# Kernel tuning notes

Measured on AMD Instinct MI355X. Metric: run time of the kernel, lower is better.

The kernel has to match this reference:

```python
import jax, jax.numpy as jnp
from jax import lax
import numpy as np

B, T = 16, 96      # sentences per batch, EDUs per document
K = 64             # kcluster
D = 768            # BERT_DIM
H = 400            # n_lstm_hidden
L = 3              # n_lstm_layers
M = 500            # n_mlp_arc
NEG = -1e9


def setup_inputs() -> dict:
    key = jax.random.key(0)
    ks = jax.random.split(key, 16)
    s = 0.1
    return {
        "embed_table": jax.random.normal(ks[0], (K, D), jnp.float32) * s,
        "multinomial": jax.random.normal(ks[1], (K, K), jnp.float32) * s,
        "wih0": jax.random.normal(ks[2], (2, 4 * H, D), jnp.float32) * s,
        "wih": jax.random.normal(ks[3], (L - 1, 2, 4 * H, 2 * H), jnp.float32) * s,
        "whh": jax.random.normal(ks[4], (L, 2, 4 * H, H), jnp.float32) * s,
        "b": jax.random.normal(ks[5], (L, 2, 4 * H), jnp.float32) * s,
        "mlp_h_w": jax.random.normal(ks[6], (M, 2 * H), jnp.float32) * s,
        "mlp_h_b": jax.random.normal(ks[7], (M,), jnp.float32) * s,
        "mlp_d_w": jax.random.normal(ks[8], (M, 2 * H), jnp.float32) * s,
        "mlp_d_b": jax.random.normal(ks[9], (M,), jnp.float32) * s,
        "biaffine_w": jax.random.normal(ks[10], (M, M), jnp.float32) * s,
        "kmeans_labels": jax.random.randint(ks[11], (B, T), 0, K),
        "heads": jax.random.randint(ks[12], (B, T - 1), 0, T),
    }


def _lse(x, axis):
    m = jnp.max(x, axis=axis, keepdims=True)
    return jnp.squeeze(m, axis) + jnp.log(jnp.sum(jnp.exp(x - m), axis=axis))


def _lstm_dir(x, Wih, Whh, bias, reverse):
    # x: [B, T, in] -> [B, T, H]; torch gate order i,f,g,o; bias = b_ih + b_hh
    xs = jnp.swapaxes(x, 0, 1)

    def step(carry, xt):
        h, c = carry
        g = xt @ Wih.T + h @ Whh.T + bias
        i, f, gg, o = jnp.split(g, 4, axis=-1)
        c = jax.nn.sigmoid(f) * c + jax.nn.sigmoid(i) * jnp.tanh(gg)
        h = jax.nn.sigmoid(o) * jnp.tanh(c)
        return (h, c), h

    z = jnp.zeros((x.shape[0], Whh.shape[1]), x.dtype)
    _, hs = lax.scan(step, (z, z), xs, reverse=reverse)
    return jnp.swapaxes(hs, 0, 1)


def _inside(s):
    # Eisner first-order inside algorithm in the log semiring.
    # s[h, d] = log-score of arc h -> d. Returns log-partition.
    n = s.shape[0]
    eye = jnp.eye(n, dtype=bool)
    C_r = jnp.where(eye, 0.0, NEG)  # complete, head on left
    C_l = jnp.where(eye, 0.0, NEG)  # complete, head on right
    I_r = jnp.full((n, n), NEG)
    I_l = jnp.full((n, n), NEG)
    for w in range(1, n):
        i = jnp.arange(n - w)
        j = i + w
        r = jnp.arange(w)
        ii = i[:, None]
        # incomplete spans: split k in [i, j-1]
        inc = _lse(C_r[ii, ii + r] + C_l[ii + r + 1, j[:, None]], axis=1)
        I_r = I_r.at[i, j].set(inc + s[i, j])
        I_l = I_l.at[i, j].set(inc + s[j, i])
        # complete right: split k in [i+1, j]
        rr = jnp.arange(1, w + 1)
        cr = _lse(I_r[ii, ii + rr] + C_r[ii + rr, j[:, None]], axis=1)
        C_r = C_r.at[i, j].set(cr)
        # complete left: split k in [i, j-1]
        cl = _lse(C_l[ii, ii + r] + I_l[ii + r, j[:, None]], axis=1)
        C_l = C_l.at[i, j].set(cl)
    return C_r[0, n - 1]


def reference(embed_table, multinomial, wih0, wih, whh, b, mlp_h_w, mlp_h_b,
              mlp_d_w, mlp_d_b, biaffine_w, kmeans_labels, heads):
    # embed lookup of kmeans cluster labels (word_embed=False branch)
    x = embed_table[kmeans_labels]  # [B, T, D]
    # 3-layer BiLSTM (eval mode: dropout = identity)
    for l in range(L):
        Wf = wih0[0] if l == 0 else wih[l - 1, 0]
        Wb = wih0[1] if l == 0 else wih[l - 1, 1]
        hf = _lstm_dir(x, Wf, whh[l, 0], b[l, 0], reverse=False)
        hb = _lstm_dir(x, Wb, whh[l, 1], b[l, 1], reverse=True)
        x = jnp.concatenate([hf, hb], axis=-1)  # [B, T, 2H]
    # arc MLPs (LeakyReLU(0.1) as in the biaffine parser MLP)
    arc_h = jax.nn.leaky_relu(x @ mlp_h_w.T + mlp_h_b, 0.1)
    arc_d = jax.nn.leaky_relu(x @ mlp_d_w.T + mlp_d_b, 0.1)
    # biaffine arc scores: s_arc[b, dep, head]
    s_arc = jnp.einsum('bxi,ij,byj->bxy', arc_d, biaffine_w, arc_h)
    # encoder_p[b, head, dep] = log_softmax over heads, then permute(0,2,1)
    p = jnp.swapaxes(jax.nn.log_softmax(s_arc, axis=-1), 1, 2)
    # reconstruction weight from raw multinomial over cluster labels
    rec = multinomial[kmeans_labels[:, :, None], kmeans_labels[:, None, :]]
    joint = p + rec  # [B, T, T]
    # score of the given (gold) tree: heads[b, d-1] -> d for deps 1..T-1
    deps = jnp.arange(1, T)
    best_score = joint[jnp.arange(B)[:, None], heads, deps[None, :]].sum(axis=1)
    # Eisner log-partition per sentence over encoder_p
    partition = jax.vmap(_inside)(p)
    # supervised loss: mean of -(best_score - partition)
    return jnp.mean(partition - best_score)
```

## Files before the change

kernel.cpp:

```cpp
#include <hip/hip_runtime.h>
#include <cmath>

#define DEV __device__ __forceinline__


#define NBLK_LSTM 400

DEV float wred_max(float v){ for(int o=32;o;o>>=1) v=fmaxf(v,__shfl_xor(v,o)); return v; }
DEV float wred_sum(float v){ for(int o=32;o;o>>=1) v+=__shfl_xor(v,o); return v; }
DEV float sigf(float x){ return 1.f/(1.f+__expf(-x)); }

DEV float agent_ld(const float* p){
  return __hip_atomic_load(p, __ATOMIC_RELAXED, __HIP_MEMORY_SCOPE_AGENT);
}
DEV void agent_st(float* p, float v){
  __hip_atomic_store(p, v, __ATOMIC_RELAXED, __HIP_MEMORY_SCOPE_AGENT);
}

__global__ __launch_bounds__(256) void embed_kern(const float* __restrict__ tab,
                                                  const int* __restrict__ labels,
                                                  float* __restrict__ x0){
  long idx = (long)blockIdx.x*256 + threadIdx.x;
  if (idx >= 1536L*768) return;
  int m = (int)(idx/768), d = (int)(idx%768);
  x0[idx] = tab[(long)labels[m]*768 + d];
}

__global__ __launch_bounds__(256) void trans_sq(const float* __restrict__ w,
                                                float* __restrict__ wt){
  int idx = blockIdx.x*256 + threadIdx.x;
  if (idx >= 250000) return;
  int j = idx/500, i = idx%500;
  wt[idx] = w[(long)i*500 + j];
}

__global__ __launch_bounds__(256) void gemm_abt(const float* __restrict__ A,
                                                const float* __restrict__ Bm,
                                                float* __restrict__ C,
                                                const float* __restrict__ bias,
                                                int M, int N, int K,
                                                long sA, long sB, long sC, int leaky){
  A  += (long)blockIdx.z * sA;
  Bm += (long)blockIdx.z * sB;
  C  += (long)blockIdx.z * sC;
  __shared__ float As[16][68];
  __shared__ float Bs[16][68];
  int tid = threadIdx.x;
  int tx = tid & 15, ty = tid >> 4;
  int m0 = blockIdx.x * 64, n0 = blockIdx.y * 64;
  int lrow = tid >> 2, lc = (tid & 3) * 4;
  float acc[4][4] = {};
  for (int k0 = 0; k0 < K; k0 += 16) {
    #pragma unroll
    for (int u = 0; u < 4; u++) {
      int k = k0 + lc + u;
      int am = m0 + lrow;
      As[lc+u][lrow] = (am < M && k < K) ? A[(long)am*K + k] : 0.f;
      int bn = n0 + lrow;
      Bs[lc+u][lrow] = (bn < N && k < K) ? Bm[(long)bn*K + k] : 0.f;
    }
    __syncthreads();
    #pragma unroll
    for (int kk = 0; kk < 16; kk++) {
      float a[4], bb[4];
      #pragma unroll
      for (int u=0;u<4;u++){ a[u]=As[kk][ty*4+u]; bb[u]=Bs[kk][tx*4+u]; }
      #pragma unroll
      for (int i=0;i<4;i++)
        #pragma unroll
        for (int j=0;j<4;j++) acc[i][j] = fmaf(a[i], bb[j], acc[i][j]);
    }
    __syncthreads();
  }
  #pragma unroll
  for (int i=0;i<4;i++){
    int m = m0 + ty*4 + i;
    if (m >= M) continue;
    #pragma unroll
    for (int j=0;j<4;j++){
      int n = n0 + tx*4 + j;
      if (n >= N) continue;
      float v = acc[i][j];
      if (bias) v += bias[n];
      if (leaky) v = v > 0.f ? v : 0.1f*v;
      C[(long)m*N + n] = v;
    }
  }
}

__global__ __launch_bounds__(256) void gemm128(const float* __restrict__ A,
                                               const float* __restrict__ Bm,
                                               float* __restrict__ C,
                                               const float* __restrict__ bias,
                                               int M, int N, int K, int leaky){
  __shared__ float As[16][132];
  __shared__ float Bs[16][132];
  int tid = threadIdx.x;
  int tx = tid & 15, ty = tid >> 4;
  int m0 = blockIdx.x*128, n0 = blockIdx.y*128;
  int lr = tid >> 1, lq = (tid & 1)*8;
  const float* Arow = A + (size_t)(m0+lr)*K + lq;
  const float* Brow = Bm + (size_t)(n0+lr)*K + lq;
  bool bok = (n0 + lr) < N;
  float acc[8][8] = {};
  for (int k0 = 0; k0 < K; k0 += 16){
    if (k0 + 16 <= K){
      float4 a0 = *(const float4*)(Arow + k0);
      float4 a1 = *(const float4*)(Arow + k0 + 4);
      float4 b0 = {0,0,0,0}, b1 = {0,0,0,0};
      if (bok){ b0 = *(const float4*)(Brow + k0); b1 = *(const float4*)(Brow + k0 + 4); }
      As[lq+0][lr]=a0.x; As[lq+1][lr]=a0.y; As[lq+2][lr]=a0.z; As[lq+3][lr]=a0.w;
      As[lq+4][lr]=a1.x; As[lq+5][lr]=a1.y; As[lq+6][lr]=a1.z; As[lq+7][lr]=a1.w;
      Bs[lq+0][lr]=b0.x; Bs[lq+1][lr]=b0.y; Bs[lq+2][lr]=b0.z; Bs[lq+3][lr]=b0.w;
      Bs[lq+4][lr]=b1.x; Bs[lq+5][lr]=b1.y; Bs[lq+6][lr]=b1.z; Bs[lq+7][lr]=b1.w;
    } else {
      #pragma unroll
      for (int u = 0; u < 8; u++){
        int k = k0 + lq + u;
        As[lq+u][lr] = (k < K) ? Arow[k0+u] : 0.f;
        Bs[lq+u][lr] = (bok && k < K) ? Brow[k0+u] : 0.f;
      }
    }
    __syncthreads();
    #pragma unroll
    for (int kk = 0; kk < 16; kk++){
      float4 a0 = *(const float4*)&As[kk][ty*8];
      float4 a1 = *(const float4*)&As[kk][ty*8+4];
      float4 b0 = *(const float4*)&Bs[kk][tx*8];
      float4 b1 = *(const float4*)&Bs[kk][tx*8+4];
      float av[8] = {a0.x,a0.y,a0.z,a0.w,a1.x,a1.y,a1.z,a1.w};
      float bv[8] = {b0.x,b0.y,b0.z,b0.w,b1.x,b1.y,b1.z,b1.w};
      #pragma unroll
      for (int i=0;i<8;i++)
        #pragma unroll
        for (int j=0;j<8;j++) acc[i][j] = fmaf(av[i], bv[j], acc[i][j]);
    }
    __syncthreads();
  }
  bool full = (n0 + 128 <= N);
  #pragma unroll
  for (int i = 0; i < 8; i++){
    int m = m0 + ty*8 + i;
    float* Crow = C + (size_t)m*N;
    if (full){
      float4 v0, v1;
      float* p0 = &v0.x; float* p1 = &v1.x;
      #pragma unroll
      for (int j = 0; j < 4; j++){
        int n = n0 + tx*8 + j;
        float v = acc[i][j];
        if (bias) v += bias[n];
        if (leaky) v = v > 0.f ? v : 0.1f*v;
        p0[j] = v;
      }
      #pragma unroll
      for (int j = 4; j < 8; j++){
        int n = n0 + tx*8 + j;
        float v = acc[i][j];
        if (bias) v += bias[n];
        if (leaky) v = v > 0.f ? v : 0.1f*v;
        p1[j-4] = v;
      }
      *(float4*)(Crow + n0 + tx*8)     = v0;
      *(float4*)(Crow + n0 + tx*8 + 4) = v1;
    } else {
      #pragma unroll
      for (int j = 0; j < 8; j++){
        int n = n0 + tx*8 + j;
        if (n < N){
          float v = acc[i][j];
          if (bias) v += bias[n];
          if (leaky) v = v > 0.f ? v : 0.1f*v;
          Crow[n] = v;
        }
      }
    }
  }
}

__global__ __launch_bounds__(128) void lstm_grid(const float* __restrict__ G,
                                                 const float* __restrict__ whh,
                                                 float* __restrict__ xout,
                                                 float* __restrict__ hbufG,
                                                 unsigned* __restrict__ flags,
                                                 int layer){
  __shared__ float Wl[32*404];
  __shared__ float hl[4*404];
  __shared__ float gb[32][5];
  int tid = threadIdx.x;
  int bid = blockIdx.x;
  int dir     = bid / 200;
  int quarter = (bid / 50) % 4;
  int slice   = bid % 50;
  int jj0  = slice * 8;
  int bat0 = quarter * 4;
  int fbase = dir*200 + quarter*50;
  const float* whhL = whh + (size_t)(layer*2 + dir)*1600*400;
  for (int i = tid; i < 3200; i += 128){
    int r = i/100, k4 = i%100;
    int g = r>>3, jjr = r&7;
    float4 v = *(const float4*)(whhL + (size_t)(g*400 + jj0 + jjr)*400 + k4*4);
    *(float4*)&Wl[r*404 + k4*4] = v;
  }
  for (int i = tid; i < 4*404; i += 128) hl[i] = 0.f;
  int ks   = (tid>>2)&15;
  int rowg = (tid&3) | ((tid>>6)<<2);
  const float* hb = hl;
  const float* wb = Wl + rowg*4*404;
  int ebl = (tid>>3)&3;
  int ejj = tid & 7;
  int ebat = bat0 + ebl;
  const float* gbase = G + (size_t)ebat*96*3200 + dir*1600 + jj0 + ejj;
  float* xo = xout + (size_t)ebat*96*800 + dir*400 + jj0 + ejj;
  float c = 0.f;
  float g0=0.f, g1=0.f, g2=0.f, g3=0.f;
  if (tid < 32){
    const float* gp0 = gbase + (size_t)(dir ? 95 : 0)*3200;
    g0 = gp0[0]; g1 = gp0[400]; g2 = gp0[800]; g3 = gp0[1200];
  }
  __syncthreads();
  for (int s = 0; s < 96; s++){
    int t = dir ? 95 - s : s;
    float acc[4][4] = {};
    #pragma unroll
    for (int q = 0; q < 6; ++q){
      int k4 = q*16 + ks;
      float4 h0 = *(const float4*)&hb[0*404 + k4*4];
      float4 h1 = *(const float4*)&hb[1*404 + k4*4];
      float4 h2 = *(const float4*)&hb[2*404 + k4*4];
      float4 h3 = *(const float4*)&hb[3*404 + k4*4];
      float4 w0 = *(const float4*)&wb[0*404 + k4*4];
      float4 w1 = *(const float4*)&wb[1*404 + k4*4];
      float4 w2 = *(const float4*)&wb[2*404 + k4*4];
      float4 w3 = *(const float4*)&wb[3*404 + k4*4];
      #pragma unroll
      for (int bi=0; bi<4; bi++){
        float4 hq = bi==0?h0: bi==1?h1: bi==2?h2: h3;
        #pragma unroll
        for (int ri=0; ri<4; ri++){
          float4 wq = ri==0?w0: ri==1?w1: ri==2?w2: w3;
          acc[bi][ri] = fmaf(hq.x,wq.x, fmaf(hq.y,wq.y,
                        fmaf(hq.z,wq.z, fmaf(hq.w,wq.w, acc[bi][ri]))));
        }
      }
    }
    if (ks < 4){
      int k4 = 96 + ks;
      float4 h0 = *(const float4*)&hb[0*404 + k4*4];
      float4 h1 = *(const float4*)&hb[1*404 + k4*4];
      float4 h2 = *(const float4*)&hb[2*404 + k4*4];
      float4 h3 = *(const float4*)&hb[3*404 + k4*4];
      float4 w0 = *(const float4*)&wb[0*404 + k4*4];
      float4 w1 = *(const float4*)&wb[1*404 + k4*4];
      float4 w2 = *(const float4*)&wb[2*404 + k4*4];
      float4 w3 = *(const float4*)&wb[3*404 + k4*4];
      #pragma unroll
      for (int bi=0; bi<4; bi++){
        float4 hq = bi==0?h0: bi==1?h1: bi==2?h2: h3;
        #pragma unroll
        for (int ri=0; ri<4; ri++){
          float4 wq = ri==0?w0: ri==1?w1: ri==2?w2: w3;
          acc[bi][ri] = fmaf(hq.x,wq.x, fmaf(hq.y,wq.y,
                        fmaf(hq.z,wq.z, fmaf(hq.w,wq.w, acc[bi][ri]))));
        }
      }
    }
    #pragma unroll
    for (int bi=0; bi<4; bi++)
      #pragma unroll
      for (int ri=0; ri<4; ri++){
        float v = acc[bi][ri];
        v += __shfl_xor(v, 4);
        v += __shfl_xor(v, 8);
        v += __shfl_xor(v, 16);
        v += __shfl_xor(v, 32);
        acc[bi][ri] = v;
      }
    if (ks == 0){
      #pragma unroll
      for (int ri=0; ri<4; ri++)
        #pragma unroll
        for (int bi=0; bi<4; bi++)
          gb[rowg*4+ri][bi] = acc[bi][ri];
    }
    __syncthreads();
    int par = s & 1;
    if (tid < 32){
      float ai = gb[     ejj][ebl] + g0;
      float af = gb[ 8 + ejj][ebl] + g1;
      float ag = gb[16 + ejj][ebl] + g2;
      float ao = gb[24 + ejj][ebl] + g3;
      c = sigf(af)*c + sigf(ai)*tanhf(ag);
      float hv = sigf(ao)*tanhf(c);
      agent_st(&hbufG[((size_t)(par*2 + dir)*16 + ebat)*400 + jj0 + ejj], hv);
      xo[(size_t)t*800] = hv;
    }
    if (s < 95){
      unsigned target = (unsigned)(layer*95 + s + 1);
      __syncthreads();
      if (tid == 0)
        __hip_atomic_store(&flags[bid*16], target, __ATOMIC_RELAXED,
                           __HIP_MEMORY_SCOPE_AGENT);
      if (tid < 32){
        int tn = dir ? 94 - s : s + 1;
        const float* gp = gbase + (size_t)tn*3200;
        g0 = gp[0]; g1 = gp[400]; g2 = gp[800]; g3 = gp[1200];
      }
      if (tid < 50){
        while (__hip_atomic_load(&flags[(fbase + tid)*16], __ATOMIC_RELAXED,
                                 __HIP_MEMORY_SCOPE_AGENT) < target){
          __builtin_amdgcn_s_sleep(1);
        }
      }
      __syncthreads();
      const float* hsrc = hbufG + (size_t)(par*2 + dir)*6400 + bat0*400;
      float hA[4], hB[4], hC[4], hT;
      #pragma unroll
      for (int bat = 0; bat < 4; bat++){
        hA[bat] = agent_ld(hsrc + bat*400 + tid);
        hB[bat] = agent_ld(hsrc + bat*400 + 128 + tid);
        hC[bat] = agent_ld(hsrc + bat*400 + 256 + tid);
      }
      hT = (tid < 64) ? agent_ld(hsrc + (tid>>4)*400 + 384 + (tid&15)) : 0.f;
      #pragma unroll
      for (int bat = 0; bat < 4; bat++){
        hl[bat*404 + tid]       = hA[bat];
        hl[bat*404 + 128 + tid] = hB[bat];
        hl[bat*404 + 256 + tid] = hC[bat];
      }
      if (tid < 64) hl[(tid>>4)*404 + 384 + (tid&15)] = hT;
      __syncthreads();
    }
  }
}

__global__ __launch_bounds__(256) void softmax_p(const float* __restrict__ sarc,
                                                 float* __restrict__ p){
  int row  = blockIdx.x*4 + (threadIdx.x >> 6);
  int lane = threadIdx.x & 63;
  int b = row/96, x = row%96;
  const float* s = sarc + (long)(b*96 + x)*96;
  float v1 = s[lane];
  float v2 = (lane+64 < 96) ? s[lane+64] : -INFINITY;
  float mx = wred_max(fmaxf(v1,v2));
  float sm = wred_sum(__expf(v1-mx) + __expf(v2-mx));
  float lse = mx + __logf(sm);
  float* pr = p + (long)b*9216;
  pr[lane*96 + x] = v1 - lse;
  if (lane+64 < 96) pr[(lane+64)*96 + x] = v2 - lse;
}

__global__ __launch_bounds__(128) void best_kern(const float* __restrict__ p,
                                                 const float* __restrict__ multinomial,
                                                 const int* __restrict__ labels,
                                                 const int* __restrict__ heads,
                                                 float* __restrict__ best){
  int b = blockIdx.x, tid = threadIdx.x;
  float acc = 0.f;
  for (int ti = tid; ti < 95; ti += 128) {
    int y = heads[b*95 + ti];
    int x = ti + 1;
    acc += p[(long)b*9216 + y*96 + x]
         + multinomial[(long)labels[b*96 + y]*64 + labels[b*96 + x]];
  }
  acc = wred_sum(acc);
  __shared__ float tmp[2];
  if ((tid & 63) == 0) tmp[tid >> 6] = acc;
  __syncthreads();
  if (tid == 0) best[b] = tmp[0] + tmp[1];
}

__global__ __launch_bounds__(1024) void inside_kern(const float* __restrict__ p,
                                                    float* __restrict__ part){
  __shared__ float Cp[96][97];
  __shared__ float Ipp[96][97];
  __shared__ float Xp[96][97];
  __shared__ float Pl[96][97];
  int b = blockIdx.x;
  const float* pB = p + (long)b*9216;
  int tid = threadIdx.x;
  for (int idx = tid; idx < 96*97; idx += 1024) {
    int row = idx/97, col = idx%97;
    float d = (row == col) ? 0.f : -1e9f;
    Cp[row][col] = d;
    Xp[row][col] = d;
    Ipp[row][col] = -1e9f;
  }
  for (int idx = tid; idx < 9216; idx += 1024)
    Pl[idx/96][idx%96] = pB[idx];
  __syncthreads();
  int g = tid >> 3, l = tid & 7;
  for (int w = 1; w < 96; w++){
    int n = 96 - w;
    if (g < n){
      int i = g, j = i + w;
      const float* pa  = &Cp[i][i];
      const float* pb2 = &Cp[j][i+1];
      float vb[12]; float m = -1e30f;
      #pragma unroll
      for (int k = 0; k < 12; k++){
        vb[k] = -1e30f;
        if (k*8 < w){
          int r = l + k*8;
          if (r < w){ float v = pa[r] + pb2[r]; vb[k] = v; m = fmaxf(m, v); }
        }
      }
      m = fmaxf(m, __shfl_xor(m,1));
      m = fmaxf(m, __shfl_xor(m,2));
      m = fmaxf(m, __shfl_xor(m,4));
      float s = 0.f;
      #pragma unroll
      for (int k = 0; k < 12; k++){
        if (k*8 < w) s += __expf(vb[k] - m);
      }
      s += __shfl_xor(s,1); s += __shfl_xor(s,2); s += __shfl_xor(s,4);
      if (l == 0){
        float inc = m + __logf(s);
        Ipp[i][j] = inc + Pl[i][j];
        Ipp[j][i] = inc + Pl[j][i];
      }
    }
    __syncthreads();
    for (int task = g; task < 2*n; task += 128){
      int typ = task < n ? 1 : 0;
      int i = typ ? task : task - n;
      int j = i + w;
      const float* pa  = typ ? &Ipp[i][i+1] : &Xp[i][i];
      const float* pb2 = typ ? &Xp[j][i+1]  : &Ipp[j][i];
      float vb[12]; float m = -1e30f;
      #pragma unroll
      for (int k = 0; k < 12; k++){
        vb[k] = -1e30f;
        if (k*8 < w){
          int r = l + k*8;
          if (r < w){ float v = pa[r] + pb2[r]; vb[k] = v; m = fmaxf(m, v); }
        }
      }
      m = fmaxf(m, __shfl_xor(m,1));
      m = fmaxf(m, __shfl_xor(m,2));
      m = fmaxf(m, __shfl_xor(m,4));
      float s = 0.f;
      #pragma unroll
      for (int k = 0; k < 12; k++){
        if (k*8 < w) s += __expf(vb[k] - m);
      }
      s += __shfl_xor(s,1); s += __shfl_xor(s,2); s += __shfl_xor(s,4);
      if (l == 0){
        float res = m + __logf(s);
        if (typ){ Cp[i][j] = res; Xp[j][i] = res; }
        else    { Cp[j][i] = res; Xp[i][j] = res; }
      }
    }
    __syncthreads();
  }
  if (tid == 0) part[b] = Cp[0][95];
}

__global__ __launch_bounds__(64) void final_kern(const float* __restrict__ part,
                                                 const float* __restrict__ best,
                                                 float* __restrict__ out){
  int lane = threadIdx.x;
  float v = (lane < 16) ? part[lane] - best[lane] : 0.f;
  v = wred_sum(v);
  if (lane == 0) out[0] = v * (1.f/16.f);
}

extern "C" void kernel_launch(void* const* d_in, const int* in_sizes, int n_in,
                              void* d_out, int out_size, void* d_ws, size_t ws_size,
                              hipStream_t stream) {
  const float* emb   = (const float*)d_in[0];
  const float* multi = (const float*)d_in[1];
  const float* wih0  = (const float*)d_in[2];
  const float* wih   = (const float*)d_in[3];
  const float* whh   = (const float*)d_in[4];
  const float* bias  = (const float*)d_in[5];
  const float* mhw   = (const float*)d_in[6];
  const float* mhb   = (const float*)d_in[7];
  const float* mdw   = (const float*)d_in[8];
  const float* mdb   = (const float*)d_in[9];
  const float* biaf  = (const float*)d_in[10];
  const int*   labels= (const int*)d_in[11];
  const int*   heads = (const int*)d_in[12];
  float* out = (float*)d_out;

  float* ws = (float*)d_ws;
  size_t off = 0;
  auto alloc = [&](size_t n){ float* q = ws + off; off += n; return q; };
  float* G    = alloc(1536L*3200);
  float* x0   = alloc(1536L*768);
  float* xA   = alloc(1536L*800);
  float* xB   = alloc(1536L*800);
  float* WTb  = alloc(500L*500);
  float* arcH = alloc(1536L*500);
  float* arcD = alloc(1536L*500);
  float* tmp  = alloc(1536L*500);
  float* sarc = alloc(16L*96*96);
  float* pbuf = alloc(16L*96*96);
  float* hbufG= alloc(2L*2*16*400);
  unsigned* flags = (unsigned*)alloc(NBLK_LSTM*16);
  float* part = alloc(16);
  float* best = alloc(16);
  (void)ws_size; (void)in_sizes; (void)n_in; (void)out_size;

  hipMemsetAsync(flags, 0, NBLK_LSTM*16*sizeof(unsigned), stream);

  embed_kern<<<(1536*768)/256, 256, 0, stream>>>(emb, labels, x0);
  trans_sq<<<(250000+255)/256, 256, 0, stream>>>(biaf, WTb);

  const float* xin = x0;
  float* xout = xA;
  for (int l = 0; l < 3; l++) {
    int Kd = (l==0) ? 768 : 800;
    const float* W = (l==0) ? wih0 : wih + (size_t)(l-1)*2*1600*800;
    gemm128<<<dim3(12,25), 256, 0, stream>>>(xin, W, G, bias + l*3200,
                                             1536, 3200, Kd, 0);
    lstm_grid<<<NBLK_LSTM, 128, 0, stream>>>(G, whh, xout, hbufG, flags, l);
    xin = xout;
    xout = (l==0) ? xB : xA;
  }
  gemm128<<<dim3(12,4), 256, 0, stream>>>(xin,  mhw, arcH, mhb, 1536, 500, 800, 1);
  gemm128<<<dim3(12,4), 256, 0, stream>>>(xin,  mdw, arcD, mdb, 1536, 500, 800, 1);
  gemm128<<<dim3(12,4), 256, 0, stream>>>(arcD, WTb, tmp, nullptr, 1536, 500, 500, 0);
  dim3 gs(2, 2, 16);
  gemm_abt<<<gs, 256, 0, stream>>>(tmp, arcH, sarc, nullptr, 96, 96, 500,
                                   96L*500, 96L*500, 96L*96, 0);
  softmax_p<<<384, 256, 0, stream>>>(sarc, pbuf);
  best_kern<<<16, 128, 0, stream>>>(pbuf, multi, labels, heads, best);
  inside_kern<<<16, 1024, 0, stream>>>(pbuf, part);
  final_kern<<<1, 64, 0, stream>>>(part, best, out);
}
```

Before: 2.272 ms.

## Pipeline per-slice flag waits in LSTM recurrence and retile arc MLP GEMMs

The LSTM step's cross-block barrier is restructured so each wavefront waits only on the producer flags for the hidden-state slice it is about to load, instead of 50 threads spinning before a block-wide barrier. Flag publishing now uses an explicit s_waitcnt on the storing wave in place of a __syncthreads, and the xout store is moved after the flag signal. This removes barriers from the 96-step serial critical path. Separately, the three arc MLP/biaffine GEMMs switch from gemm128 on a 12x4 grid to gemm_abt on a 24x8 grid, giving more blocks for these small GEMMs. The risk is subtle memory-ordering issues in the relaxed flag protocol.

Result: slower. 2.416 ms (+6.3%).

```diff
diff --git a/kernel.cpp b/kernel.cpp
--- a/kernel.cpp
+++ b/kernel.cpp
@@ -15,6 +15,9 @@
 }
 DEV void agent_st(float* p, float v){
   __hip_atomic_store(p, v, __ATOMIC_RELAXED, __HIP_MEMORY_SCOPE_AGENT);
+}
+DEV unsigned flag_ld(const unsigned* p){
+  return __hip_atomic_load(p, __ATOMIC_RELAXED, __HIP_MEMORY_SCOPE_AGENT);
 }
 
 __global__ __launch_bounds__(256) void embed_kern(const float* __restrict__ tab,
@@ -218,6 +221,10 @@
     const float* gp0 = gbase + (size_t)(dir ? 95 : 0)*3200;
     g0 = gp0[0]; g1 = gp0[400]; g2 = gp0[800]; g3 = gp0[1200];
   }
+  const unsigned* fl0 = flags + (size_t)(fbase + (tid>>3))*16;
+  const unsigned* fl1 = flags + (size_t)(fbase + 16 + (tid>>3))*16;
+  const unsigned* fl2 = flags + (size_t)(fbase + 32 + (tid>>3))*16;
+  const unsigned* flt = flags + (size_t)(fbase + 48 + ((tid&15)>>3))*16;
   __syncthreads();
   for (int s = 0; s < 96; s++){
     int t = dir ? 95 - s : s;
@@ -285,43 +292,49 @@
     }
     __syncthreads();
     int par = s & 1;
+    unsigned target = (unsigned)(layer*95 + s + 1);
+    float hv = 0.f;
     if (tid < 32){
       float ai = gb[     ejj][ebl] + g0;
       float af = gb[ 8 + ejj][ebl] + g1;
       float ag = gb[16 + ejj][ebl] + g2;
       float ao = gb[24 + ejj][ebl] + g3;
       c = sigf(af)*c + sigf(ai)*tanhf(ag);
-      float hv = sigf(ao)*tanhf(c);
-      agent_st(&hbufG[((size_t)(par*2 + dir)*16 + ebat)*400 + jj0 + ejj], hv);
-      xo[(size_t)t*800] = hv;
-    }
-    if (s < 95){
-      unsigned target = (unsigned)(layer*95 + s + 1);
-      __syncthreads();
+      hv = sigf(ao)*tanhf(c);
+      if (s < 95)
+        agent_st(&hbufG[((size_t)(par*2 + dir)*16 + ebat)*400 + jj0 + ejj], hv);
+    }
+    if (s < 95 && tid < 64){
+      asm volatile("s_waitcnt vmcnt(0)" ::: "memory");
       if (tid == 0)
         __hip_atomic_store(&flags[bid*16], target, __ATOMIC_RELAXED,
                            __HIP_MEMORY_SCOPE_AGENT);
-      if (tid < 32){
+    }
+    if (tid < 32){
+      xo[(size_t)t*800] = hv;
+      if (s < 95){
         int tn = dir ? 94 - s : s + 1;
         const float* gp = gbase + (size_t)tn*3200;
         g0 = gp[0]; g1 = gp[400]; g2 = gp[800]; g3 = gp[1200];
       }
-      if (tid < 50){
-        while (__hip_atomic_load(&flags[(fbase + tid)*16], __ATOMIC_RELAXED,
-                                 __HIP_MEMORY_SCOPE_AGENT) < target){
-          __builtin_amdgcn_s_sleep(1);
-        }
-      }
-      __syncthreads();
+    }
+    if (s < 95){
       const float* hsrc = hbufG + (size_t)(par*2 + dir)*6400 + bat0*400;
       float hA[4], hB[4], hC[4], hT;
-      #pragma unroll
-      for (int bat = 0; bat < 4; bat++){
-        hA[bat] = agent_ld(hsrc + bat*400 + tid);
-        hB[bat] = agent_ld(hsrc + bat*400 + 128 + tid);
-        hC[bat] = agent_ld(hsrc + bat*400 + 256 + tid);
-      }
-      hT = (tid < 64) ? agent_ld(hsrc + (tid>>4)*400 + 384 + (tid&15)) : 0.f;
+      while (flag_ld(fl0) < target) __builtin_amdgcn_s_sleep(1);
+      #pragma unroll
+      for (int bat = 0; bat < 4; bat++) hA[bat] = agent_ld(hsrc + bat*400 + tid);
+      while (flag_ld(fl1) < target) __builtin_amdgcn_s_sleep(1);
+      #pragma unroll
+      for (int bat = 0; bat < 4; bat++) hB[bat] = agent_ld(hsrc + bat*400 + 128 + tid);
+      while (flag_ld(fl2) < target) __builtin_amdgcn_s_sleep(1);
+      #pragma unroll
+      for (int bat = 0; bat < 4; bat++) hC[bat] = agent_ld(hsrc + bat*400 + 256 + tid);
+      hT = 0.f;
+      if (tid < 64){
+        while (flag_ld(flt) < target) __builtin_amdgcn_s_sleep(1);
+        hT = agent_ld(hsrc + (tid>>4)*400 + 384 + (tid&15));
+      }
       #pragma unroll
       for (int bat = 0; bat < 4; bat++){
         hl[bat*404 + tid]       = hA[bat];
@@ -329,8 +342,8 @@
         hl[bat*404 + 256 + tid] = hC[bat];
       }
       if (tid < 64) hl[(tid>>4)*404 + 384 + (tid&15)] = hT;
-      __syncthreads();
-    }
+    }
+    __syncthreads();
   }
 }
 
@@ -518,9 +531,10 @@
     xin = xout;
     xout = (l==0) ? xB : xA;
   }
-  gemm128<<<dim3(12,4), 256, 0, stream>>>(xin,  mhw, arcH, mhb, 1536, 500, 800, 1);
-  gemm128<<<dim3(12,4), 256, 0, stream>>>(xin,  mdw, arcD, mdb, 1536, 500, 800, 1);
-  gemm128<<<dim3(12,4), 256, 0, stream>>>(arcD, WTb, tmp, nullptr, 1536, 500, 500, 0);
+  dim3 gm(24, 8, 1);
+  gemm_abt<<<gm, 256, 0, stream>>>(xin,  mhw, arcH, mhb, 1536, 500, 800, 0,0,0, 1);
+  gemm_abt<<<gm, 256, 0, stream>>>(xin,  mdw, arcD, mdb, 1536, 500, 800, 0,0,0, 1);
+  gemm_abt<<<gm, 256, 0, stream>>>(arcD, WTb, tmp, nullptr, 1536, 500, 500, 0,0,0, 0);
   dim3 gs(2, 2, 16);
   gemm_abt<<<gs, 256, 0, stream>>>(tmp, arcH, sarc, nullptr, 96, 96, 500,
                                    96L*500, 96L*500, 96L*96, 0);
```
